# Kernel tuning notes

Hardware: AMD Instinct MI355X
Metric: run time of the kernel (lower is better)

## Reference

```python
import jax, jax.numpy as jnp
import numpy as np
from jax import lax

T, B, NPG, F_IN = 10, 8, 1080, 2
N = B * NPG            # 8640 nodes total
DEG = 16
E = N * DEG            # 138240 edges
HID, HEADS = 64, 8
LSTM_H, OUT = 128, 2
NEG_SLOPE = 0.2

# (in_dim, heads, out_channels_per_head) for the 4 GATConv layers
LAYER_DIMS = [(F_IN, HEADS, HID), (HID * HEADS, HEADS, HID // 2),
              (HID // 2 * HEADS, HEADS, HID // 4), (HID // 4 * HEADS, 1, HID // 8)]


def setup_inputs() -> dict:
    key = jax.random.key(0)
    ks = iter(jax.random.split(key, 40))
    inp = {}
    inp['x_seq'] = jax.random.normal(next(ks), (T, N, F_IN), jnp.float32)
    # kNN-style edges within each graph: every node receives DEG random in-graph neighbors
    dst = jnp.repeat(jnp.arange(N, dtype=jnp.int32), DEG)
    offs = (dst // NPG) * NPG
    src = offs + jax.random.randint(next(ks), (E,), 0, NPG, jnp.int32)
    inp['edge_index'] = jnp.stack([src, dst])
    inp['batch'] = jnp.repeat(jnp.arange(B, dtype=jnp.int32), NPG)
    # GAT params: W [in, H*C], att_src/att_dst [H, C], bias [H*C]
    for li, (fin, h, c) in enumerate(LAYER_DIMS, start=1):
        s = 1.0 / np.sqrt(fin)
        inp[f'W{li}'] = jax.random.uniform(next(ks), (fin, h * c), jnp.float32, -s, s)
        inp[f'as{li}'] = jax.random.uniform(next(ks), (h, c), jnp.float32, -s, s)
        inp[f'ad{li}'] = jax.random.uniform(next(ks), (h, c), jnp.float32, -s, s)
        inp[f'b{li}'] = jnp.zeros((h * c,), jnp.float32)
    # LSTM (PyTorch layout, gate order i,f,g,o)
    gdim = HID // 8
    sl = 1.0 / np.sqrt(LSTM_H)
    inp['w_ih'] = jax.random.uniform(next(ks), (4 * LSTM_H, gdim), jnp.float32, -sl, sl)
    inp['w_hh'] = jax.random.uniform(next(ks), (4 * LSTM_H, LSTM_H), jnp.float32, -sl, sl)
    inp['b_ih'] = jax.random.uniform(next(ks), (4 * LSTM_H,), jnp.float32, -sl, sl)
    inp['b_hh'] = jax.random.uniform(next(ks), (4 * LSTM_H,), jnp.float32, -sl, sl)
    inp['w_fc'] = jax.random.uniform(next(ks), (OUT, LSTM_H), jnp.float32, -sl, sl)
    inp['b_fc'] = jax.random.uniform(next(ks), (OUT,), jnp.float32, -sl, sl)
    return inp


def _forward(x_seq, W1, as1, ad1, b1, W2, as2, ad2, b2, W3, as3, ad3, b3,
             W4, as4, ad4, b4, w_ih, w_hh, b_ih, b_hh, w_fc, b_fc,
             edge_index, batch):
    # PyG GATConv adds self-loops by default
    loops = jnp.arange(N, dtype=edge_index.dtype)
    src = jnp.concatenate([edge_index[0], loops])
    dst = jnp.concatenate([edge_index[1], loops])

    def gat(x, W, a_s, a_d, b):
        Hh, C = a_s.shape
        h = (x @ W).reshape(N, Hh, C)                 # [N,H,C]
        e_s = (h * a_s).sum(-1)                        # [N,H]
        e_d = (h * a_d).sum(-1)
        e = jax.nn.leaky_relu(e_s[src] + e_d[dst], NEG_SLOPE)   # [Etot,H]
        m = jax.ops.segment_max(e, dst, num_segments=N)
        ex = jnp.exp(e - m[dst])
        den = jax.ops.segment_sum(ex, dst, num_segments=N)
        alpha = ex / (den[dst] + 1e-16)
        out = jax.ops.segment_sum(h[src] * alpha[:, :, None], dst, num_segments=N)
        return out.reshape(N, Hh * C) + b

    counts = jax.ops.segment_sum(jnp.ones((N,), jnp.float32), batch, num_segments=B)[:, None]

    def per_t(x):  # eval mode: dropout = identity
        x = jax.nn.elu(gat(x, W1, as1, ad1, b1))
        x = jax.nn.elu(gat(x, W2, as2, ad2, b2))
        x = jax.nn.elu(gat(x, W3, as3, ad3, b3))
        x = jax.nn.elu(gat(x, W4, as4, ad4, b4))
        return jax.ops.segment_sum(x, batch, num_segments=B) / counts  # mean pool [B, hid//8]

    _, embs = lax.scan(lambda c, xt: (c, per_t(xt)), None, x_seq)  # [T,B,gdim]

    h0 = jnp.zeros((B, LSTM_H), x_seq.dtype)
    c0 = jnp.zeros((B, LSTM_H), x_seq.dtype)

    def step(carry, xt):
        h, c = carry
        g = xt @ w_ih.T + h @ w_hh.T + b_ih + b_hh
        i, f, gg, o = jnp.split(g, 4, axis=-1)
        c = jax.nn.sigmoid(f) * c + jax.nn.sigmoid(i) * jnp.tanh(gg)
        h = jax.nn.sigmoid(o) * jnp.tanh(c)
        return (h, c), None

    (h_last, _), _ = lax.scan(step, (h0, c0), embs)
    return h_last @ w_fc.T + b_fc  # [B, OUT] (eval path: last timestep only)


def reference(x_seq, W1, as1, ad1, b1, W2, as2, ad2, b2, W3, as3, ad3, b3,
              W4, as4, ad4, b4, w_ih, w_hh, b_ih, b_hh, w_fc, b_fc,
              edge_index, batch):
    return _forward(x_seq, W1, as1, ad1, b1, W2, as2, ad2, b2, W3, as3, ad3, b3,
                    W4, as4, ad4, b4, w_ih, w_hh, b_ih, b_hh, w_fc, b_fc,
                    edge_index, batch)
```

## Files before the change

kernel.cpp:

```cpp
#include <hip/hip_runtime.h>
#include <math.h>

#define T_TOT 10
#define NB    8
#define NPG   1080
#define NN    (NB*NPG)
#define DEG   16

typedef unsigned short ushortT;
using short8 = __attribute__((ext_vector_type(8))) short;
using f32x4  = __attribute__((ext_vector_type(4))) float;

__device__ __forceinline__ float lrelu(float v) { return v > 0.f ? v : 0.2f*v; }
__device__ __forceinline__ float elu1(float v)  { return v > 0.f ? v : (__expf(v) - 1.f); }
__device__ __forceinline__ float bf2f(ushortT h){ return __uint_as_float(((unsigned)h) << 16); }
__device__ __forceinline__ float bfl(unsigned u){ return __uint_as_float(u << 16); }
__device__ __forceinline__ float bfh(unsigned u){ return __uint_as_float(u & 0xFFFF0000u); }
__device__ __forceinline__ ushortT rne(float v) {
    unsigned u = __float_as_uint(v);
    u += 0x7FFFu + ((u >> 16) & 1u);
    return (ushortT)(u >> 16);
}
__device__ __forceinline__ unsigned pk2(float a, float b) {
    return (unsigned)rne(a) | ((unsigned)rne(b) << 16);
}
__device__ __forceinline__ int xswz(int b, int nwg) {
    int q = nwg >> 3, r = nwg & 7;
    int x = b & 7, i = b >> 3;
    return x*q + min(x, r) + i;
}
__device__ __forceinline__ void gld16(const void* g, void* lbase, int laneoff) {
#if __has_builtin(__builtin_amdgcn_global_load_lds)
    typedef __attribute__((address_space(1))) const unsigned int GU;
    typedef __attribute__((address_space(3))) unsigned int LU;
    __builtin_amdgcn_global_load_lds((GU*)g, (LU*)lbase, 16, 0, 0);
    (void)laneoff;
#else
    *(uint4*)((char*)lbase + laneoff) = *(const uint4*)g;
#endif
}

__global__ void k_prep_l1(const float* __restrict__ W1, const float* __restrict__ as1,
                          const float* __restrict__ ad1, float* __restrict__ A) {
    int tid = threadIdx.x;
    if (tid >= 32) return;
    int h = tid & 7, k = (tid >> 3) & 1, sd = tid >> 4;
    const float* att = sd ? ad1 : as1;
    float acc = 0.f;
    for (int c = 0; c < 64; ++c) acc += W1[k*512 + h*64 + c] * att[h*64 + c];
    A[sd*16 + k*8 + h] = acc;
}

__global__ void k_prepW(const float* __restrict__ W, ushortT* __restrict__ WT, int K, int M) {
    int i = blockIdx.x*256 + threadIdx.x;
    if (i >= K*M) return;
    int k = i / M, m = i - k*M;
    WT[(size_t)m*K + k] = rne(W[i]);
}

__global__ __launch_bounds__(256) void k_gat1(
    const float* __restrict__ x, const int* __restrict__ esrc,
    const float* __restrict__ A, const float* __restrict__ W1,
    const float* __restrict__ b1, ushortT* __restrict__ q, int R) {
    int tid = threadIdx.x;
    int g = xswz(blockIdx.x, gridDim.x)*32 + (tid >> 3);
    int l = tid & 7;
    if (g >= R*8) g = R*8 - 1;
    int r = g >> 3, hh = g & 7;
    int t = r / NN, n = r - t*NN;
    float2 xr = *(const float2*)&x[2*r];
    float As0 = A[hh], As1 = A[8+hh];
    float edv = xr.x*A[16+hh] + xr.y*A[24+hh];
    float ev[3], xs0[3], xs1[3];
    float m = -1e30f;
    #pragma unroll
    for (int s = 0; s < 3; ++s) {
        int j = s*8 + l;
        if (j < 17) {
            int src = (j == 16) ? r : (t*NN + esrc[n*DEG + j]);
            float2 xs = *(const float2*)&x[2*src];
            xs0[s] = xs.x; xs1[s] = xs.y;
            float e = lrelu(xs.x*As0 + xs.y*As1 + edv);
            ev[s] = e; m = fmaxf(m, e);
        } else { ev[s] = -1e30f; xs0[s] = 0.f; xs1[s] = 0.f; }
    }
    #pragma unroll
    for (int off = 4; off >= 1; off >>= 1) m = fmaxf(m, __shfl_xor(m, off, 8));
    float den = 0.f, p0 = 0.f, p1 = 0.f;
    #pragma unroll
    for (int s = 0; s < 3; ++s) {
        float e2 = __expf(ev[s] - m);
        den += e2; p0 += e2*xs0[s]; p1 += e2*xs1[s];
    }
    #pragma unroll
    for (int off = 4; off >= 1; off >>= 1) {
        den += __shfl_xor(den, off, 8);
        p0  += __shfl_xor(p0,  off, 8);
        p1  += __shfl_xor(p1,  off, 8);
    }
    float inv = 1.f/(den + 1e-16f);
    float xa0 = p0*inv, xa1 = p1*inv;
    int col = hh*64 + l*8;
    float4 w0a = *(const float4*)&W1[col],       w0b = *(const float4*)&W1[col+4];
    float4 w1a = *(const float4*)&W1[512+col],   w1b = *(const float4*)&W1[512+col+4];
    float4 bba = *(const float4*)&b1[col],       bbb = *(const float4*)&b1[col+4];
    float v0 = elu1(xa0*w0a.x + xa1*w1a.x + bba.x);
    float v1 = elu1(xa0*w0a.y + xa1*w1a.y + bba.y);
    float v2 = elu1(xa0*w0a.z + xa1*w1a.z + bba.z);
    float v3 = elu1(xa0*w0a.w + xa1*w1a.w + bba.w);
    float v4 = elu1(xa0*w0b.x + xa1*w1b.x + bbb.x);
    float v5 = elu1(xa0*w0b.y + xa1*w1b.y + bbb.y);
    float v6 = elu1(xa0*w0b.z + xa1*w1b.z + bbb.z);
    float v7 = elu1(xa0*w0b.w + xa1*w1b.w + bbb.w);
    uint4 o;
    o.x = pk2(v0,v1); o.y = pk2(v2,v3); o.z = pk2(v4,v5); o.w = pk2(v6,v7);
    *(uint4*)&q[(size_t)r*512 + col] = o;
}

template<int H, int C, int LANES, bool BFIN, bool BFOUT>
__global__ __launch_bounds__(256) void k_gat(
    const void* __restrict__ hb_, const int* __restrict__ esrc,
    const float* __restrict__ es, const float* __restrict__ ed,
    const float* __restrict__ bias, float* __restrict__ out,
    ushortT* __restrict__ ohi, int R) {
    constexpr int CPL = C/LANES;
    constexpr int GPB = 256/LANES;
    constexpr int EPL = (17 + LANES - 1)/LANES;
    constexpr int HC = H*C;
    int tid = threadIdx.x;
    int l = tid & (LANES-1);
    int g = xswz(blockIdx.x, gridDim.x)*GPB + tid/LANES;
    if (g >= R*H) g = R*H - 1;
    int r = g / H, hh = g % H;
    int t = r / NN, n = r - t*NN;
    float edv = ed[(size_t)r*H + hh];
    float ev[EPL]; int sv[EPL];
    float m = -1e30f;
    #pragma unroll
    for (int s = 0; s < EPL; ++s) {
        int j = s*LANES + l;
        if (j < 17) {
            int src = (j == 16) ? r : (t*NN + esrc[n*DEG + j]);
            sv[s] = src;
            float e = lrelu(es[(size_t)src*H + hh] + edv);
            ev[s] = e; m = fmaxf(m, e);
        } else { ev[s] = -1e30f; sv[s] = r; }
    }
    #pragma unroll
    for (int off = LANES/2; off >= 1; off >>= 1) m = fmaxf(m, __shfl_xor(m, off, LANES));
    float den = 0.f;
    float wv[EPL];
    #pragma unroll
    for (int s = 0; s < EPL; ++s) {
        float e2 = __expf(ev[s] - m);
        wv[s] = e2; den += e2;
    }
    #pragma unroll
    for (int off = LANES/2; off >= 1; off >>= 1) den += __shfl_xor(den, off, LANES);
    float inv = 1.f/(den + 1e-16f);
    #pragma unroll
    for (int s = 0; s < EPL; ++s) wv[s] *= inv;

    int lb = (tid & 63) & ~(LANES-1);
    float acc[CPL] = {};
    #pragma unroll
    for (int j = 0; j < 17; ++j) {
        float wj = __shfl(wv[j/LANES], lb + (j & (LANES-1)), 64);
        int   sj = __shfl(sv[j/LANES], lb + (j & (LANES-1)), 64);
        if constexpr (BFIN) {
            const ushortT* hp = (const ushortT*)hb_ + (size_t)sj*HC + hh*C + l*CPL;
            uint4 hv = *(const uint4*)hp;
            acc[0] += wj*bfl(hv.x); acc[1] += wj*bfh(hv.x);
            acc[2] += wj*bfl(hv.y); acc[3] += wj*bfh(hv.y);
            acc[4] += wj*bfl(hv.z); acc[5] += wj*bfh(hv.z);
            acc[6] += wj*bfl(hv.w); acc[7] += wj*bfh(hv.w);
        } else {
            const float* hp = (const float*)hb_ + (size_t)sj*HC + hh*C + l*CPL;
            float4 hv = *(const float4*)hp;
            acc[0] += wj*hv.x; acc[1] += wj*hv.y;
            acc[2] += wj*hv.z; acc[3] += wj*hv.w;
        }
    }
    int base = hh*C + l*CPL;
    #pragma unroll
    for (int c = 0; c < CPL; ++c) acc[c] = elu1(acc[c] + bias[base + c]);
    if constexpr (BFOUT) {
        uint4 o;
        o.x = pk2(acc[0],acc[1]); o.y = pk2(acc[2],acc[3]);
        o.z = pk2(acc[4],acc[5]); o.w = pk2(acc[6],acc[7]);
        *(uint4*)&ohi[(size_t)r*HC + base] = o;
    } else {
        *(float4*)&out[(size_t)r*HC + base] = make_float4(acc[0],acc[1],acc[2],acc[3]);
    }
}

template<int C>
__global__ __launch_bounds__(512) void k_gemm_mfma(
    const ushortT* __restrict__ X, const ushortT* __restrict__ WT,
    const float* __restrict__ as_, const float* __restrict__ ad_,
    ushortT* __restrict__ Hout, float* __restrict__ es, float* __restrict__ ed,
    int R, int K, int M) {
    __shared__ __align__(16) char smem[65536];
    int tid = threadIdx.x;
    int wid = tid >> 6, l = tid & 63;
    int l15 = l & 15, lg = l >> 4;
    int wr = wid >> 2, wc = wid & 3;
    int rb = blockIdx.x*128, cb = blockIdx.y*128;
    const size_t strideB = (size_t)K*2;
    const int nKT = K >> 6;

    f32x4 acc[4][2] = {};
    int aoff[4], asw[4], boff[2], bsw[2];
    #pragma unroll
    for (int i = 0; i < 4; ++i) {
        int ar = wr*64 + i*16 + l15;
        aoff[i] = ar*128; asw[i] = (ar & 7) << 4;
    }
    #pragma unroll
    for (int j = 0; j < 2; ++j) {
        int bc = wc*32 + j*16 + l15;
        boff[j] = 16384 + bc*128; bsw[j] = (bc & 7) << 4;
    }
    int kb0 = lg*16;
    int srow = tid >> 3;
    int colb = ((tid & 7)*16) ^ ((srow & 7) << 4);

    auto stage = [&](int buf, int kt) {
        int kbyte = kt*128;
        char* base = smem + (buf << 15);
        #pragma unroll
        for (int i = 0; i < 2; ++i) {
            int row = i*64 + srow;
            const char* sa = (const char*)X  + (size_t)min(rb + row, R - 1)*strideB + kbyte + colb;
            const char* sb = (const char*)WT + (size_t)(cb + row)*strideB + kbyte + colb;
            int dst = (i*64 + wid*8)*128;
            gld16(sa, base + dst,         l*16);
            gld16(sb, base + 16384 + dst, l*16);
        }
    };

    stage(0, 0);
    __syncthreads();
    for (int kt = 0; kt < nKT; ++kt) {
        int cur = kt & 1;
        if (kt + 1 < nKT) stage(cur ^ 1, kt + 1);
        const char* bufp = smem + (cur << 15);
        #pragma unroll
        for (int ks = 0; ks < 2; ++ks) {
            int kb = ks*64 + kb0;
            short8 ah[4], bv[2];
            #pragma unroll
            for (int i = 0; i < 4; ++i)
                ah[i] = *(const short8*)(bufp + aoff[i] + (kb ^ asw[i]));
            #pragma unroll
            for (int j = 0; j < 2; ++j)
                bv[j] = *(const short8*)(bufp + boff[j] + (kb ^ bsw[j]));
            #pragma unroll
            for (int mt = 0; mt < 4; ++mt)
                #pragma unroll
                for (int nt = 0; nt < 2; ++nt)
                    acc[mt][nt] = __builtin_amdgcn_mfma_f32_16x16x32_bf16(ah[mt], bv[nt], acc[mt][nt], 0, 0, 0);
        }
        __syncthreads();
    }
    constexpr int NSL = 128/C;
    constexpr int NHW = 32/C;
    int hg0 = cb / C;
    float asv[2], adv[2];
    #pragma unroll
    for (int nt = 0; nt < 2; ++nt) {
        int col = wc*32 + nt*16 + l15;
        int h = col / C, c = col - h*C;
        asv[nt] = as_[(hg0 + h)*C + c];
        adv[nt] = ad_[(hg0 + h)*C + c];
    }
    float* ebp = (float*)smem;
    #pragma unroll
    for (int mt = 0; mt < 4; ++mt) {
        float ps[4][NHW] = {}, pd[4][NHW] = {};
        #pragma unroll
        for (int nt = 0; nt < 2; ++nt) {
            int sl = (nt*16)/C;
            #pragma unroll
            for (int q = 0; q < 4; ++q) {
                ps[q][sl] += acc[mt][nt][q]*asv[nt];
                pd[q][sl] += acc[mt][nt][q]*adv[nt];
            }
        }
        #pragma unroll
        for (int off = 1; off < 16; off <<= 1)
            #pragma unroll
            for (int q = 0; q < 4; ++q)
                #pragma unroll
                for (int sl = 0; sl < NHW; ++sl) {
                    ps[q][sl] += __shfl_xor(ps[q][sl], off);
                    pd[q][sl] += __shfl_xor(pd[q][sl], off);
                }
        if (l15 == 0) {
            #pragma unroll
            for (int q = 0; q < 4; ++q) {
                int row = wr*64 + mt*16 + lg*4 + q;
                #pragma unroll
                for (int sl = 0; sl < NHW; ++sl) {
                    ebp[(row*NSL + wc*NHW + sl)*2 + 0] = ps[q][sl];
                    ebp[(row*NSL + wc*NHW + sl)*2 + 1] = pd[q][sl];
                }
            }
        }
        #pragma unroll
        for (int nt = 0; nt < 2; ++nt) {
            int col = cb + wc*32 + nt*16 + l15;
            #pragma unroll
            for (int q = 0; q < 4; ++q) {
                int r = rb + wr*64 + mt*16 + lg*4 + q;
                if (r < R) Hout[(size_t)r*M + col] = rne(acc[mt][nt][q]);
            }
        }
    }
    __syncthreads();
    for (int i = tid; i < 128*NSL; i += 512) {
        int row = i / NSL, sl = i - row*NSL;
        int r = rb + row;
        if (r < R) {
            es[(size_t)r*8 + hg0 + sl] = ebp[i*2 + 0];
            ed[(size_t)r*8 + hg0 + sl] = ebp[i*2 + 1];
        }
    }
}

__global__ __launch_bounds__(256) void k_lin4(
    const ushortT* __restrict__ X, const float* __restrict__ W,
    const float* __restrict__ as_, const float* __restrict__ ad_,
    float* __restrict__ Hout, float* __restrict__ es, float* __restrict__ ed, int R) {
    int tid = threadIdx.x;
    int l = tid & 7;
    int r = blockIdx.x*32 + (tid >> 3);
    if (r >= R) return;
    const ushortT* xp = X + (size_t)r*128 + l*16;
    uint4 a = *(const uint4*)xp;
    uint4 b = *(const uint4*)(xp + 8);
    float xv[16];
    xv[0]=bfl(a.x); xv[1]=bfh(a.x); xv[2]=bfl(a.y); xv[3]=bfh(a.y);
    xv[4]=bfl(a.z); xv[5]=bfh(a.z); xv[6]=bfl(a.w); xv[7]=bfh(a.w);
    xv[8]=bfl(b.x); xv[9]=bfh(b.x); xv[10]=bfl(b.y); xv[11]=bfh(b.y);
    xv[12]=bfl(b.z); xv[13]=bfh(b.z); xv[14]=bfl(b.w); xv[15]=bfh(b.w);
    float acc[8] = {};
    #pragma unroll
    for (int kk = 0; kk < 16; ++kk) {
        const float* wr = W + (l*16 + kk)*8;
        float4 wa = *(const float4*)wr, wb = *(const float4*)(wr + 4);
        acc[0] += xv[kk]*wa.x; acc[1] += xv[kk]*wa.y;
        acc[2] += xv[kk]*wa.z; acc[3] += xv[kk]*wa.w;
        acc[4] += xv[kk]*wb.x; acc[5] += xv[kk]*wb.y;
        acc[6] += xv[kk]*wb.z; acc[7] += xv[kk]*wb.w;
    }
    #pragma unroll
    for (int off = 4; off >= 1; off >>= 1)
        #pragma unroll
        for (int c = 0; c < 8; ++c) acc[c] += __shfl_xor(acc[c], off, 8);
    if (l == 0) {
        *(float4*)&Hout[(size_t)r*8]     = make_float4(acc[0],acc[1],acc[2],acc[3]);
        *(float4*)&Hout[(size_t)r*8 + 4] = make_float4(acc[4],acc[5],acc[6],acc[7]);
        float ps = 0.f, pd = 0.f;
        #pragma unroll
        for (int c = 0; c < 8; ++c) { ps += acc[c]*as_[c]; pd += acc[c]*ad_[c]; }
        es[r] = ps; ed[r] = pd;
    }
}

__global__ void k_pool(const float* __restrict__ x4, float* __restrict__ emb, int t0) {
    __shared__ float red[256];
    int tl = blockIdx.x >> 3, b = blockIdx.x & 7;
    int tid = threadIdx.x;
    int c = tid & 7, nl = tid >> 3;
    float s = 0.f;
    for (int k = 0; k < 34; ++k) {
        int n = nl + 32*k;
        if (n < NPG) s += x4[((size_t)tl*NN + b*NPG + n)*8 + c];
    }
    red[tid] = s;
    __syncthreads();
    for (int st = 16; st >= 1; st >>= 1) {
        if (nl < st) red[tid] += red[tid + st*8];
        __syncthreads();
    }
    if (nl == 0) emb[((t0 + tl)*8 + b)*8 + c] = red[c] * (1.f/1080.f);
}

__global__ __launch_bounds__(512) void k_lstm(
    const float* __restrict__ emb, const float* __restrict__ w_ih,
    const float* __restrict__ w_hh, const float* __restrict__ b_ih,
    const float* __restrict__ b_hh, const float* __restrict__ w_fc,
    const float* __restrict__ b_fc, float* __restrict__ out) {
    int b = blockIdx.x, u = threadIdx.x;
    __shared__ float h[128], cst[128], g[512], eall[T_TOT*8];
    if (u < 128) { h[u] = 0.f; cst[u] = 0.f; }
    if (u < T_TOT*8) eall[u] = emb[((u >> 3)*8 + b)*8 + (u & 7)];
    float wreg[128];
    {
        const float* wp = w_hh + (size_t)u*128;
        #pragma unroll
        for (int k4 = 0; k4 < 32; ++k4) {
            float4 v = *(const float4*)&wp[k4*4];
            wreg[4*k4+0] = v.x; wreg[4*k4+1] = v.y;
            wreg[4*k4+2] = v.z; wreg[4*k4+3] = v.w;
        }
    }
    float wih[8];
    #pragma unroll
    for (int k = 0; k < 8; ++k) wih[k] = w_ih[(size_t)u*8 + k];
    float bsum = b_ih[u] + b_hh[u];
    __syncthreads();
    for (int t = 0; t < T_TOT; ++t) {
        float a0 = bsum, a1 = 0.f, a2 = 0.f, a3 = 0.f;
        #pragma unroll
        for (int k = 0; k < 8; ++k) a0 += eall[t*8 + k]*wih[k];
        #pragma unroll
        for (int k = 0; k < 32; ++k) {
            a0 += h[4*k+0]*wreg[4*k+0];
            a1 += h[4*k+1]*wreg[4*k+1];
            a2 += h[4*k+2]*wreg[4*k+2];
            a3 += h[4*k+3]*wreg[4*k+3];
        }
        g[u] = (a0 + a1) + (a2 + a3);
        __syncthreads();
        if (u < 128) {
            float ig = 1.f/(1.f + __expf(-g[u]));
            float fg = 1.f/(1.f + __expf(-g[128+u]));
            float gg = tanhf(g[256+u]);
            float og = 1.f/(1.f + __expf(-g[384+u]));
            float cn = fg*cst[u] + ig*gg;
            cst[u] = cn;
            h[u] = og*tanhf(cn);
        }
        __syncthreads();
    }
    if (u < 64) {
        float p0 = h[u]*w_fc[u]       + h[u+64]*w_fc[64+u];
        float p1 = h[u]*w_fc[128+u]   + h[u+64]*w_fc[192+u];
        #pragma unroll
        for (int off = 32; off >= 1; off >>= 1) {
            p0 += __shfl_xor(p0, off, 64);
            p1 += __shfl_xor(p1, off, 64);
        }
        if (u == 0) {
            out[b*2 + 0] = p0 + b_fc[0];
            out[b*2 + 1] = p1 + b_fc[1];
        }
    }
}

extern "C" void kernel_launch(void* const* d_in, const int* in_sizes, int n_in,
                              void* d_out, int out_size, void* d_ws, size_t ws_size,
                              hipStream_t stream) {
    const float* x_seq = (const float*)d_in[0];
    const int*   edge  = (const int*)d_in[1];
    const float* W1 = (const float*)d_in[3];
    const float* as1 = (const float*)d_in[4];
    const float* ad1 = (const float*)d_in[5];
    const float* b1  = (const float*)d_in[6];
    const float* W2 = (const float*)d_in[7];
    const float* as2 = (const float*)d_in[8];
    const float* ad2 = (const float*)d_in[9];
    const float* b2  = (const float*)d_in[10];
    const float* W3 = (const float*)d_in[11];
    const float* as3 = (const float*)d_in[12];
    const float* ad3 = (const float*)d_in[13];
    const float* b3  = (const float*)d_in[14];
    const float* W4 = (const float*)d_in[15];
    const float* as4 = (const float*)d_in[16];
    const float* ad4 = (const float*)d_in[17];
    const float* b4  = (const float*)d_in[18];
    const float* w_ih = (const float*)d_in[19];
    const float* w_hh = (const float*)d_in[20];
    const float* b_ih = (const float*)d_in[21];
    const float* b_hh = (const float*)d_in[22];
    const float* w_fc = (const float*)d_in[23];
    const float* b_fc = (const float*)d_in[24];

    char* w = (char*)d_ws;
    auto alloc = [&](size_t bytes) {
        char* p = w; w += (bytes + 255) & ~(size_t)255; return p;
    };
    float*   A1  = (float*)alloc(128);
    float*   emb = (float*)alloc((size_t)T_TOT*8*8*4);
    ushortT* W2T = (ushortT*)alloc((size_t)256*512*2);
    ushortT* W3T = (ushortT*)alloc((size_t)128*256*2);
    size_t used = (size_t)(w - (char*)d_ws);
    size_t perT = (size_t)NN*(1024 + 512 + 512 + 256 + 256 + 128);
    size_t rem = (ws_size > used + 4096) ? ws_size - used - 4096 : 0;
    int Tc = (int)(rem / perT);
    if (Tc > T_TOT) Tc = T_TOT;
    if (Tc < 1) Tc = 1;
    ushortT* Q  = (ushortT*)alloc((size_t)Tc*NN*1024);
    ushortT* P  = (ushortT*)alloc((size_t)Tc*NN*512);
    ushortT* G3 = (ushortT*)alloc((size_t)Tc*NN*512);
    ushortT* H3 = (ushortT*)alloc((size_t)Tc*NN*256);
    ushortT* G4 = (ushortT*)alloc((size_t)Tc*NN*256);
    float*   ES = (float*)alloc((size_t)Tc*NN*32);
    float*   ED = (float*)alloc((size_t)Tc*NN*32);
    float*   P4 = (float*)alloc((size_t)Tc*NN*32);
    float*   G5 = (float*)alloc((size_t)Tc*NN*32);

    k_prep_l1<<<1, 64, 0, stream>>>(W1, as1, ad1, A1);
    k_prepW<<<(256*512 + 255)/256, 256, 0, stream>>>(W2, W2T, 512, 256);
    k_prepW<<<(128*256 + 255)/256, 256, 0, stream>>>(W3, W3T, 256, 128);

    for (int t0 = 0; t0 < T_TOT; t0 += Tc) {
        int tc = (Tc < T_TOT - t0) ? Tc : (T_TOT - t0);
        int R = tc*NN;
        int nrb = (R + 127)/128;
        const float* xoff = x_seq + (size_t)t0*NN*2;
        k_gat1<<<(R*8 + 31)/32, 256, 0, stream>>>(xoff, edge, A1, W1, b1, Q, R);
        k_gemm_mfma<32><<<dim3(nrb, 2), 512, 0, stream>>>(Q, W2T, as2, ad2, P, ES, ED, R, 512, 256);
        k_gat<8,32,4,true,true><<<(R*8 + 63)/64, 256, 0, stream>>>(P, edge, ES, ED, b2, nullptr, G3, R);
        k_gemm_mfma<16><<<dim3(nrb, 1), 512, 0, stream>>>(G3, W3T, as3, ad3, H3, ES, ED, R, 256, 128);
        k_gat<8,16,2,true,true><<<(R*8 + 127)/128, 256, 0, stream>>>(H3, edge, ES, ED, b3, nullptr, G4, R);
        k_lin4<<<(R + 31)/32, 256, 0, stream>>>(G4, W4, as4, ad4, P4, ES, ED, R);
        k_gat<1,8,2,false,false><<<(R + 127)/128, 256, 0, stream>>>(P4, edge, ES, ED, b4, G5, nullptr, R);
        k_pool<<<tc*8, 256, 0, stream>>>(G5, emb, t0);
    }
    k_lstm<<<8, 512, 0, stream>>>(emb, w_ih, w_hh, b_ih, b_hh, w_fc, b_fc, (float*)d_out);
}
```

Before: 389.4 us.

## Deepen MFMA GEMM pipeline to 4-stage async LDS loads with manual waitcnt

The bf16 MFMA GEMM drops its double-buffered 64-wide K tiles in favour of a 4-slot ring of 32-wide K slices, loaded with global_load_lds. Explicit vmcnt waits and raw s_barrier calls let three slices stay in flight while the current one is consumed. K becomes a template parameter so the loop can be fully specialised, the XOR swizzle is replaced by a K-chunk-major LDS layout, and s_setprio is raised around the MFMA burst. The aim is to hide global load latency behind compute. The risks are LDS bank conflicts from the unswizzled layout and the correctness of the hand-written waitcnt counts.

```diff
diff --git a/kernel.cpp b/kernel.cpp
--- a/kernel.cpp
+++ b/kernel.cpp
@@ -38,6 +38,12 @@
 #else
     *(uint4*)((char*)lbase + laneoff) = *(const uint4*)g;
 #endif
+}
+template<int N> __device__ __forceinline__ void vwait() {
+    asm volatile("s_waitcnt vmcnt(%0)" :: "i"(N) : "memory");
+}
+__device__ __forceinline__ void sbar() {
+    asm volatile("s_barrier" ::: "memory");
 }
 
 __global__ void k_prep_l1(const float* __restrict__ W1, const float* __restrict__ as1,
@@ -194,75 +200,67 @@
     }
 }
 
-template<int C>
+template<int C, int K>
 __global__ __launch_bounds__(512) void k_gemm_mfma(
     const ushortT* __restrict__ X, const ushortT* __restrict__ WT,
     const float* __restrict__ as_, const float* __restrict__ ad_,
     ushortT* __restrict__ Hout, float* __restrict__ es, float* __restrict__ ed,
-    int R, int K, int M) {
+    int R, int M) {
     __shared__ __align__(16) char smem[65536];
+    constexpr int HTOT = K/32;
     int tid = threadIdx.x;
     int wid = tid >> 6, l = tid & 63;
     int l15 = l & 15, lg = l >> 4;
     int wr = wid >> 2, wc = wid & 3;
     int rb = blockIdx.x*128, cb = blockIdx.y*128;
     const size_t strideB = (size_t)K*2;
-    const int nKT = K >> 6;
 
     f32x4 acc[4][2] = {};
-    int aoff[4], asw[4], boff[2], bsw[2];
-    #pragma unroll
-    for (int i = 0; i < 4; ++i) {
-        int ar = wr*64 + i*16 + l15;
-        aoff[i] = ar*128; asw[i] = (ar & 7) << 4;
-    }
-    #pragma unroll
-    for (int j = 0; j < 2; ++j) {
-        int bc = wc*32 + j*16 + l15;
-        boff[j] = 16384 + bc*128; bsw[j] = (bc & 7) << 4;
-    }
-    int kb0 = lg*16;
-    int srow = tid >> 3;
-    int colb = ((tid & 7)*16) ^ ((srow & 7) << 4);
-
-    auto stage = [&](int buf, int kt) {
-        int kbyte = kt*128;
-        char* base = smem + (buf << 15);
-        #pragma unroll
-        for (int i = 0; i < 2; ++i) {
-            int row = i*64 + srow;
-            const char* sa = (const char*)X  + (size_t)min(rb + row, R - 1)*strideB + kbyte + colb;
-            const char* sb = (const char*)WT + (size_t)(cb + row)*strideB + kbyte + colb;
-            int dst = (i*64 + wid*8)*128;
-            gld16(sa, base + dst,         l*16);
-            gld16(sb, base + 16384 + dst, l*16);
-        }
+    int aoff[4], boff[2];
+    #pragma unroll
+    for (int i = 0; i < 4; ++i) aoff[i] = lg*2048 + (wr*64 + i*16 + l15)*16;
+    #pragma unroll
+    for (int j = 0; j < 2; ++j) boff[j] = 8192 + lg*2048 + (wc*32 + j*16 + l15)*16;
+
+    int grow = tid & 127, gkch = tid >> 7;
+    const char* Asrc = (const char*)X  + (size_t)min(rb + grow, R - 1)*strideB + gkch*16;
+    const char* Bsrc = (const char*)WT + (size_t)(cb + grow)*strideB + gkch*16;
+    char* ldst = smem + wid*1024;
+
+    auto stage = [&](int H) {
+        int s = H & 3;
+        size_t kb = (size_t)H*64;
+        gld16(Asrc + kb, ldst + s*16384,        l*16);
+        gld16(Bsrc + kb, ldst + s*16384 + 8192, l*16);
     };
-
-    stage(0, 0);
+    auto phase = [&](int H) {
+        const char* sp = smem + (H & 3)*16384;
+        short8 ah[4], bv[2];
+        #pragma unroll
+        for (int i = 0; i < 4; ++i) ah[i] = *(const short8*)(sp + aoff[i]);
+        #pragma unroll
+        for (int j = 0; j < 2; ++j) bv[j] = *(const short8*)(sp + boff[j]);
+        __builtin_amdgcn_s_setprio(1);
+        #pragma unroll
+        for (int mt = 0; mt < 4; ++mt)
+            #pragma unroll
+            for (int nt = 0; nt < 2; ++nt)
+                acc[mt][nt] = __builtin_amdgcn_mfma_f32_16x16x32_bf16(ah[mt], bv[nt], acc[mt][nt], 0, 0, 0);
+        __builtin_amdgcn_s_setprio(0);
+    };
+
+    stage(0); stage(1); stage(2);
+    for (int H = 0; H <= HTOT - 4; ++H) {
+        stage(H + 3);
+        vwait<6>();
+        sbar();
+        phase(H);
+        sbar();
+    }
+    vwait<4>(); sbar(); phase(HTOT - 3); sbar();
+    vwait<2>(); sbar(); phase(HTOT - 2); sbar();
+    vwait<0>(); sbar(); phase(HTOT - 1); sbar();
     __syncthreads();
-    for (int kt = 0; kt < nKT; ++kt) {
-        int cur = kt & 1;
-        if (kt + 1 < nKT) stage(cur ^ 1, kt + 1);
-        const char* bufp = smem + (cur << 15);
-        #pragma unroll
-        for (int ks = 0; ks < 2; ++ks) {
-            int kb = ks*64 + kb0;
-            short8 ah[4], bv[2];
-            #pragma unroll
-            for (int i = 0; i < 4; ++i)
-                ah[i] = *(const short8*)(bufp + aoff[i] + (kb ^ asw[i]));
-            #pragma unroll
-            for (int j = 0; j < 2; ++j)
-                bv[j] = *(const short8*)(bufp + boff[j] + (kb ^ bsw[j]));
-            #pragma unroll
-            for (int mt = 0; mt < 4; ++mt)
-                #pragma unroll
-                for (int nt = 0; nt < 2; ++nt)
-                    acc[mt][nt] = __builtin_amdgcn_mfma_f32_16x16x32_bf16(ah[mt], bv[nt], acc[mt][nt], 0, 0, 0);
-        }
-        __syncthreads();
-    }
     constexpr int NSL = 128/C;
     constexpr int NHW = 32/C;
     int hg0 = cb / C;
@@ -512,9 +510,9 @@
         int nrb = (R + 127)/128;
         const float* xoff = x_seq + (size_t)t0*NN*2;
         k_gat1<<<(R*8 + 31)/32, 256, 0, stream>>>(xoff, edge, A1, W1, b1, Q, R);
-        k_gemm_mfma<32><<<dim3(nrb, 2), 512, 0, stream>>>(Q, W2T, as2, ad2, P, ES, ED, R, 512, 256);
+        k_gemm_mfma<32,512><<<dim3(nrb, 2), 512, 0, stream>>>(Q, W2T, as2, ad2, P, ES, ED, R, 256);
         k_gat<8,32,4,true,true><<<(R*8 + 63)/64, 256, 0, stream>>>(P, edge, ES, ED, b2, nullptr, G3, R);
-        k_gemm_mfma<16><<<dim3(nrb, 1), 512, 0, stream>>>(G3, W3T, as3, ad3, H3, ES, ED, R, 256, 128);
+        k_gemm_mfma<16,256><<<dim3(nrb, 1), 512, 0, stream>>>(G3, W3T, as3, ad3, H3, ES, ED, R, 128);
         k_gat<8,16,2,true,true><<<(R*8 + 127)/128, 256, 0, stream>>>(H3, edge, ES, ED, b3, nullptr, G4, R);
         k_lin4<<<(R + 31)/32, 256, 0, stream>>>(G4, W4, as4, ad4, P4, ES, ED, R);
         k_gat<1,8,2,false,false><<<(R + 127)/128, 256, 0, stream>>>(P4, edge, ES, ED, b4, G5, nullptr, R);
```

Result: slower. 398.9 us (+2.5%).

## Fuse layer-3 aggregation with layer-4 linear, and layer-4 aggregation with mean pooling

Applied to the files above, without the earlier changes.

Replaces the layer-3 GAT aggregation plus the separate lin4 kernel with one kernel. It projects the ELU output straight through W4 via a 16-lane shuffle reduction, so the bf16 G4 intermediate is never written or read back. The layer-4 aggregation is also fused with mean pooling, using shared-memory bins and global atomics into emb, which is zeroed by a memset first. This removes two launches per chunk and two intermediate buffers, at the cost of shuffle reductions, atomics and non-deterministic summation order in the pooled embeddings.

```diff
diff --git a/kernel.cpp b/kernel.cpp
--- a/kernel.cpp
+++ b/kernel.cpp
@@ -13,7 +13,6 @@
 
 __device__ __forceinline__ float lrelu(float v) { return v > 0.f ? v : 0.2f*v; }
 __device__ __forceinline__ float elu1(float v)  { return v > 0.f ? v : (__expf(v) - 1.f); }
-__device__ __forceinline__ float bf2f(ushortT h){ return __uint_as_float(((unsigned)h) << 16); }
 __device__ __forceinline__ float bfl(unsigned u){ return __uint_as_float(u << 16); }
 __device__ __forceinline__ float bfh(unsigned u){ return __uint_as_float(u & 0xFFFF0000u); }
 __device__ __forceinline__ ushortT rne(float v) {
@@ -194,6 +193,151 @@
     }
 }
 
+__global__ __launch_bounds__(256) void k_gat3_lin4(
+    const ushortT* __restrict__ hb, const int* __restrict__ esrc,
+    const float* __restrict__ es, const float* __restrict__ ed,
+    const float* __restrict__ bias, const float* __restrict__ W4,
+    const float* __restrict__ as4, const float* __restrict__ ad4,
+    float* __restrict__ H4, float* __restrict__ es4, float* __restrict__ ed4,
+    int R) {
+    int tid = threadIdx.x;
+    int l = tid & 1;
+    int g = xswz(blockIdx.x, gridDim.x)*128 + (tid >> 1);
+    if (g >= R*8) g = R*8 - 1;
+    int r = g >> 3, hh = g & 7;
+    int t = r / NN, n = r - t*NN;
+    float edv = ed[(size_t)r*8 + hh];
+    float ev[9]; int sv[9];
+    float m = -1e30f;
+    #pragma unroll
+    for (int s = 0; s < 9; ++s) {
+        int j = s*2 + l;
+        if (j < 17) {
+            int src = (j == 16) ? r : (t*NN + esrc[n*DEG + j]);
+            sv[s] = src;
+            float e = lrelu(es[(size_t)src*8 + hh] + edv);
+            ev[s] = e; m = fmaxf(m, e);
+        } else { ev[s] = -1e30f; sv[s] = r; }
+    }
+    m = fmaxf(m, __shfl_xor(m, 1, 2));
+    float den = 0.f, wv[9];
+    #pragma unroll
+    for (int s = 0; s < 9; ++s) {
+        float e2 = __expf(ev[s] - m);
+        wv[s] = e2; den += e2;
+    }
+    den += __shfl_xor(den, 1, 2);
+    float inv = 1.f/(den + 1e-16f);
+    #pragma unroll
+    for (int s = 0; s < 9; ++s) wv[s] *= inv;
+
+    int lb = (tid & 63) & ~1;
+    float acc[8] = {};
+    #pragma unroll
+    for (int j = 0; j < 17; ++j) {
+        float wj = __shfl(wv[j >> 1], lb + (j & 1), 64);
+        int   sj = __shfl(sv[j >> 1], lb + (j & 1), 64);
+        const ushortT* hp = hb + (size_t)sj*128 + hh*16 + l*8;
+        uint4 hv = *(const uint4*)hp;
+        acc[0] += wj*bfl(hv.x); acc[1] += wj*bfh(hv.x);
+        acc[2] += wj*bfl(hv.y); acc[3] += wj*bfh(hv.y);
+        acc[4] += wj*bfl(hv.z); acc[5] += wj*bfh(hv.z);
+        acc[6] += wj*bfl(hv.w); acc[7] += wj*bfh(hv.w);
+    }
+    int c0 = hh*16 + l*8;
+    #pragma unroll
+    for (int k = 0; k < 8; ++k) acc[k] = elu1(acc[k] + bias[c0 + k]);
+    float pj[8] = {};
+    #pragma unroll
+    for (int k = 0; k < 8; ++k) {
+        const float* wr = W4 + (size_t)(c0 + k)*8;
+        float4 wa = *(const float4*)wr, wb = *(const float4*)(wr + 4);
+        pj[0] += acc[k]*wa.x; pj[1] += acc[k]*wa.y;
+        pj[2] += acc[k]*wa.z; pj[3] += acc[k]*wa.w;
+        pj[4] += acc[k]*wb.x; pj[5] += acc[k]*wb.y;
+        pj[6] += acc[k]*wb.z; pj[7] += acc[k]*wb.w;
+    }
+    #pragma unroll
+    for (int off = 1; off <= 8; off <<= 1)
+        #pragma unroll
+        for (int j = 0; j < 8; ++j) pj[j] += __shfl_xor(pj[j], off, 16);
+    if ((tid & 15) == 0) {
+        *(float4*)&H4[(size_t)r*8]     = make_float4(pj[0],pj[1],pj[2],pj[3]);
+        *(float4*)&H4[(size_t)r*8 + 4] = make_float4(pj[4],pj[5],pj[6],pj[7]);
+        float ps = 0.f, pd = 0.f;
+        #pragma unroll
+        for (int j = 0; j < 8; ++j) { ps += pj[j]*as4[j]; pd += pj[j]*ad4[j]; }
+        es4[r] = ps; ed4[r] = pd;
+    }
+}
+
+__global__ __launch_bounds__(256) void k_gat4_pool(
+    const float* __restrict__ hb, const int* __restrict__ esrc,
+    const float* __restrict__ es, const float* __restrict__ ed,
+    const float* __restrict__ bias, float* __restrict__ emb,
+    int R, int t0) {
+    __shared__ float bins[2][8];
+    int tid = threadIdx.x;
+    if (tid < 16) bins[tid >> 3][tid & 7] = 0.f;
+    __syncthreads();
+    int l = tid & 1;
+    int rb0 = xswz(blockIdx.x, gridDim.x)*128;
+    int g = rb0 + (tid >> 1);
+    bool dup = false;
+    if (g >= R) { g = R - 1; dup = true; }
+    int r = g;
+    int t = r / NN, n = r - t*NN;
+    float edv = ed[r];
+    float ev[9]; int sv[9];
+    float m = -1e30f;
+    #pragma unroll
+    for (int s = 0; s < 9; ++s) {
+        int j = s*2 + l;
+        if (j < 17) {
+            int src = (j == 16) ? r : (t*NN + esrc[n*DEG + j]);
+            sv[s] = src;
+            float e = lrelu(es[src] + edv);
+            ev[s] = e; m = fmaxf(m, e);
+        } else { ev[s] = -1e30f; sv[s] = r; }
+    }
+    m = fmaxf(m, __shfl_xor(m, 1, 2));
+    float den = 0.f, wv[9];
+    #pragma unroll
+    for (int s = 0; s < 9; ++s) {
+        float e2 = __expf(ev[s] - m);
+        wv[s] = e2; den += e2;
+    }
+    den += __shfl_xor(den, 1, 2);
+    float inv = 1.f/(den + 1e-16f);
+    #pragma unroll
+    for (int s = 0; s < 9; ++s) wv[s] *= inv;
+
+    int lb = (tid & 63) & ~1;
+    float acc[4] = {};
+    #pragma unroll
+    for (int j = 0; j < 17; ++j) {
+        float wj = __shfl(wv[j >> 1], lb + (j & 1), 64);
+        int   sj = __shfl(sv[j >> 1], lb + (j & 1), 64);
+        float4 hv = *(const float4*)&hb[(size_t)sj*8 + l*4];
+        acc[0] += wj*hv.x; acc[1] += wj*hv.y;
+        acc[2] += wj*hv.z; acc[3] += wj*hv.w;
+    }
+    #pragma unroll
+    for (int c = 0; c < 4; ++c) acc[c] = elu1(acc[c] + bias[l*4 + c]);
+    if (!dup) {
+        int bin = r/NPG - rb0/NPG;
+        #pragma unroll
+        for (int c = 0; c < 4; ++c) atomicAdd(&bins[bin][l*4 + c], acc[c]);
+    }
+    __syncthreads();
+    if (tid < 16) {
+        int bin = tid >> 3, c = tid & 7;
+        int erow = rb0/NPG + bin;
+        if (erow < R/NPG)
+            atomicAdd(&emb[(t0*8 + erow)*8 + c], bins[bin][c]*(1.f/1080.f));
+    }
+}
+
 template<int C>
 __global__ __launch_bounds__(512) void k_gemm_mfma(
     const ushortT* __restrict__ X, const ushortT* __restrict__ WT,
@@ -326,65 +470,6 @@
             ed[(size_t)r*8 + hg0 + sl] = ebp[i*2 + 1];
         }
     }
-}
-
-__global__ __launch_bounds__(256) void k_lin4(
-    const ushortT* __restrict__ X, const float* __restrict__ W,
-    const float* __restrict__ as_, const float* __restrict__ ad_,
-    float* __restrict__ Hout, float* __restrict__ es, float* __restrict__ ed, int R) {
-    int tid = threadIdx.x;
-    int l = tid & 7;
-    int r = blockIdx.x*32 + (tid >> 3);
-    if (r >= R) return;
-    const ushortT* xp = X + (size_t)r*128 + l*16;
-    uint4 a = *(const uint4*)xp;
-    uint4 b = *(const uint4*)(xp + 8);
-    float xv[16];
-    xv[0]=bfl(a.x); xv[1]=bfh(a.x); xv[2]=bfl(a.y); xv[3]=bfh(a.y);
-    xv[4]=bfl(a.z); xv[5]=bfh(a.z); xv[6]=bfl(a.w); xv[7]=bfh(a.w);
-    xv[8]=bfl(b.x); xv[9]=bfh(b.x); xv[10]=bfl(b.y); xv[11]=bfh(b.y);
-    xv[12]=bfl(b.z); xv[13]=bfh(b.z); xv[14]=bfl(b.w); xv[15]=bfh(b.w);
-    float acc[8] = {};
-    #pragma unroll
-    for (int kk = 0; kk < 16; ++kk) {
-        const float* wr = W + (l*16 + kk)*8;
-        float4 wa = *(const float4*)wr, wb = *(const float4*)(wr + 4);
-        acc[0] += xv[kk]*wa.x; acc[1] += xv[kk]*wa.y;
-        acc[2] += xv[kk]*wa.z; acc[3] += xv[kk]*wa.w;
-        acc[4] += xv[kk]*wb.x; acc[5] += xv[kk]*wb.y;
-        acc[6] += xv[kk]*wb.z; acc[7] += xv[kk]*wb.w;
-    }
-    #pragma unroll
-    for (int off = 4; off >= 1; off >>= 1)
-        #pragma unroll
-        for (int c = 0; c < 8; ++c) acc[c] += __shfl_xor(acc[c], off, 8);
-    if (l == 0) {
-        *(float4*)&Hout[(size_t)r*8]     = make_float4(acc[0],acc[1],acc[2],acc[3]);
-        *(float4*)&Hout[(size_t)r*8 + 4] = make_float4(acc[4],acc[5],acc[6],acc[7]);
-        float ps = 0.f, pd = 0.f;
-        #pragma unroll
-        for (int c = 0; c < 8; ++c) { ps += acc[c]*as_[c]; pd += acc[c]*ad_[c]; }
-        es[r] = ps; ed[r] = pd;
-    }
-}
-
-__global__ void k_pool(const float* __restrict__ x4, float* __restrict__ emb, int t0) {
-    __shared__ float red[256];
-    int tl = blockIdx.x >> 3, b = blockIdx.x & 7;
-    int tid = threadIdx.x;
-    int c = tid & 7, nl = tid >> 3;
-    float s = 0.f;
-    for (int k = 0; k < 34; ++k) {
-        int n = nl + 32*k;
-        if (n < NPG) s += x4[((size_t)tl*NN + b*NPG + n)*8 + c];
-    }
-    red[tid] = s;
-    __syncthreads();
-    for (int st = 16; st >= 1; st >>= 1) {
-        if (nl < st) red[tid] += red[tid + st*8];
-        __syncthreads();
-    }
-    if (nl == 0) emb[((t0 + tl)*8 + b)*8 + c] = red[c] * (1.f/1080.f);
 }
 
 __global__ __launch_bounds__(512) void k_lstm(
@@ -487,21 +572,22 @@
     ushortT* W2T = (ushortT*)alloc((size_t)256*512*2);
     ushortT* W3T = (ushortT*)alloc((size_t)128*256*2);
     size_t used = (size_t)(w - (char*)d_ws);
-    size_t perT = (size_t)NN*(1024 + 512 + 512 + 256 + 256 + 128);
+    size_t perT = (size_t)NN*(1024 + 512 + 512 + 256 + 32 + 64 + 8 + 64);
     size_t rem = (ws_size > used + 4096) ? ws_size - used - 4096 : 0;
     int Tc = (int)(rem / perT);
     if (Tc > T_TOT) Tc = T_TOT;
     if (Tc < 1) Tc = 1;
-    ushortT* Q  = (ushortT*)alloc((size_t)Tc*NN*1024);
-    ushortT* P  = (ushortT*)alloc((size_t)Tc*NN*512);
-    ushortT* G3 = (ushortT*)alloc((size_t)Tc*NN*512);
-    ushortT* H3 = (ushortT*)alloc((size_t)Tc*NN*256);
-    ushortT* G4 = (ushortT*)alloc((size_t)Tc*NN*256);
-    float*   ES = (float*)alloc((size_t)Tc*NN*32);
-    float*   ED = (float*)alloc((size_t)Tc*NN*32);
-    float*   P4 = (float*)alloc((size_t)Tc*NN*32);
-    float*   G5 = (float*)alloc((size_t)Tc*NN*32);
-
+    ushortT* Q   = (ushortT*)alloc((size_t)Tc*NN*1024);
+    ushortT* P   = (ushortT*)alloc((size_t)Tc*NN*512);
+    ushortT* G3  = (ushortT*)alloc((size_t)Tc*NN*512);
+    ushortT* H3  = (ushortT*)alloc((size_t)Tc*NN*256);
+    float*   H4  = (float*)alloc((size_t)Tc*NN*32);
+    float*   ES  = (float*)alloc((size_t)Tc*NN*32);
+    float*   ED  = (float*)alloc((size_t)Tc*NN*32);
+    float*   ES4 = (float*)alloc((size_t)Tc*NN*4);
+    float*   ED4 = (float*)alloc((size_t)Tc*NN*4);
+
+    hipMemsetAsync(emb, 0, (size_t)T_TOT*8*8*4, stream);
     k_prep_l1<<<1, 64, 0, stream>>>(W1, as1, ad1, A1);
     k_prepW<<<(256*512 + 255)/256, 256, 0, stream>>>(W2, W2T, 512, 256);
     k_prepW<<<(128*256 + 255)/256, 256, 0, stream>>>(W3, W3T, 256, 128);
@@ -515,10 +601,8 @@
         k_gemm_mfma<32><<<dim3(nrb, 2), 512, 0, stream>>>(Q, W2T, as2, ad2, P, ES, ED, R, 512, 256);
         k_gat<8,32,4,true,true><<<(R*8 + 63)/64, 256, 0, stream>>>(P, edge, ES, ED, b2, nullptr, G3, R);
         k_gemm_mfma<16><<<dim3(nrb, 1), 512, 0, stream>>>(G3, W3T, as3, ad3, H3, ES, ED, R, 256, 128);
-        k_gat<8,16,2,true,true><<<(R*8 + 127)/128, 256, 0, stream>>>(H3, edge, ES, ED, b3, nullptr, G4, R);
-        k_lin4<<<(R + 31)/32, 256, 0, stream>>>(G4, W4, as4, ad4, P4, ES, ED, R);
-        k_gat<1,8,2,false,false><<<(R + 127)/128, 256, 0, stream>>>(P4, edge, ES, ED, b4, G5, nullptr, R);
-        k_pool<<<tc*8, 256, 0, stream>>>(G5, emb, t0);
+        k_gat3_lin4<<<(R*8 + 127)/128, 256, 0, stream>>>(H3, edge, ES, ED, b3, W4, as4, ad4, H4, ES4, ED4, R);
+        k_gat4_pool<<<(R + 127)/128, 256, 0, stream>>>(H4, edge, ES4, ED4, b4, emb, R, t0);
     }
     k_lstm<<<8, 512, 0, stream>>>(emb, w_ih, w_hh, b_ih, b_hh, w_fc, b_fc, (float*)d_out);
 }
```

Result: faster. 379.2 us (-2.6%).
